# Kernel tuning notes

Hardware: AMD Instinct MI355X
Metric: run time of the kernel (lower is better)

The kernel has to match this reference:

```python
import jax, jax.numpy as jnp
import numpy as np

B, F, H, S, K, L, C = 128, 8192, 8192, 4, 32, 3, 100  # batch, encoded feats, hidden, segments, synapses/seg, hidden layers, classes


def setup_inputs() -> dict:
    key = jax.random.key(0)
    k1, k2, k3, k4, k5, k6 = jax.random.split(key, 6)
    # binary encoded input activations (thermometer-coded tabular features)
    x = jax.random.randint(k1, (B, F), 0, 2).astype(jnp.float32)
    # sign weights in {-1,+1} for each synapse of each segment of each neuron
    signs0 = jnp.where(jax.random.bernoulli(k2, 0.5, (S, H, K)), 1.0, -1.0).astype(jnp.float32)
    signsH = jnp.where(jax.random.bernoulli(k3, 0.5, (L - 1, S, H, K)), 1.0, -1.0).astype(jnp.float32)
    # synapse source indices (irregular connectivity)
    idx0 = jax.random.randint(k4, (S, H, K), 0, F, dtype=jnp.int32)
    idxH = jax.random.randint(k5, (L - 1, S, H, K), 0, H, dtype=jnp.int32)
    # per-layer output connection matrices [L, H, C]
    wout = jax.random.normal(k6, (L, H, C), dtype=jnp.float32) * 0.02
    return {"x": x, "signs0": signs0, "signsH": signsH, "wout": wout,
            "idx0": idx0, "idxH": idxH, "threshold": 8}


def _segment_layer(a, idx, signs, threshold):
    # a: [B, P] prev activations; idx/signs: [S, H, K]
    g = a[:, idx]                                  # [B, S, H, K] irregular gather
    z = jnp.einsum('bshk,shk->bsh', g, signs)      # per-segment summed input
    fired = jnp.any(z >= threshold, axis=1)        # OR over segments -> [B, H]
    return fired.astype(a.dtype)


def reference(x, signs0, signsH, wout, idx0, idxH, threshold):
    thr = jnp.float32(threshold)
    a = _segment_layer(x, idx0, signs0, thr)       # hidden layer 0
    acts = [a]
    for l in range(idxH.shape[0]):                 # remaining hidden layers (fixed small L)
        a = _segment_layer(a, idxH[l], signsH[l], thr)
        acts.append(a)
    # sum class votes from every hidden layer's output connection matrix
    out = jnp.einsum('lbh,lhc->bc', jnp.stack(acts, 0), wout)  # [B, C]
    return out
```

## Files before the change

### kernel.cpp

```cpp
#include <hip/hip_runtime.h>
#include <stdint.h>

#define B 128
#define F 8192
#define H 8192
#define S 4
#define K 32
#define L 3
#define C 100

__global__ void pack_x_kernel(const float* __restrict__ x, uint32_t* __restrict__ xP,
                              float* __restrict__ out) {
    const int zi = blockIdx.x * 128 + threadIdx.x;
    if (zi < B * C) out[zi] = 0.0f;

    const int b = threadIdx.x;
    const int wv = threadIdx.x >> 6;
    const int f0 = blockIdx.x * 8;
    const float4* xr = (const float4*)(x + (size_t)b * F + f0);
#pragma unroll
    for (int j = 0; j < 2; ++j) {
        const float4 v = xr[j];
        const uint64_t m0 = __ballot(v.x > 0.5f);
        const uint64_t m1 = __ballot(v.y > 0.5f);
        const uint64_t m2 = __ballot(v.z > 0.5f);
        const uint64_t m3 = __ballot(v.w > 0.5f);
        if ((threadIdx.x & 63) == 0) {
            const int f = f0 + 4 * j;
            uint32_t* lo = xP + (size_t)(2 * wv) * F;
            uint32_t* hi = xP + (size_t)(2 * wv + 1) * F;
            lo[f + 0] = (uint32_t)m0;  hi[f + 0] = (uint32_t)(m0 >> 32);
            lo[f + 1] = (uint32_t)m1;  hi[f + 1] = (uint32_t)(m1 >> 32);
            lo[f + 2] = (uint32_t)m2;  hi[f + 2] = (uint32_t)(m2 >> 32);
            lo[f + 3] = (uint32_t)m3;  hi[f + 3] = (uint32_t)(m3 >> 32);
        }
    }
}

__device__ __forceinline__ int load_threshold(const int* p) {
    int v = *p;
    if (v >= (1 << 23)) v = (int)__int_as_float(v);
    return v;
}

#define ISG_STRIDE 40

__device__ __forceinline__ void layer_body(const uint32_t* __restrict__ prevP,
                                           const int* __restrict__ idx,
                                           const float* __restrict__ signs,
                                           uint32_t* __restrict__ outP,
                                           const int thr, const int bid,
                                           uint32_t* tab, uint32_t* isg,
                                           uint32_t* fbuf) {
    const int tid  = threadIdx.x;
    const int lane = tid & 63;
    const int sw   = tid >> 6;
    const int w    = bid & 3;
    const int hg   = bid >> 2;
    const int h    = hg * 64 + lane;

    {
        const int4* src = (const int4*)(prevP + (size_t)w * H);
        int4* dst = (int4*)tab;
#pragma unroll
        for (int i = 0; i < 8; ++i)
            dst[i * 256 + tid] = src[i * 256 + tid];
    }
    {
        const int hrow = tid >> 2;
        const int k0   = (tid & 3) * 8;
#pragma unroll
        for (int s = 0; s < S; ++s) {
            const int4*   ib = (const int4*)(idx   + ((size_t)s * H + hg * 64) * K);
            const float4* sb = (const float4*)(signs + ((size_t)s * H + hg * 64) * K);
            const int4   ia = ib[2 * tid],  ic = ib[2 * tid + 1];
            const float4 sa = sb[2 * tid],  sc = sb[2 * tid + 1];
            uint4* dst = (uint4*)(isg + s * (64 * ISG_STRIDE) + hrow * ISG_STRIDE + k0);
            uint4 p0, p1;
            p0.x = (uint32_t)ia.x | ((uint32_t)__float_as_int(sa.x) & 0x80000000u);
            p0.y = (uint32_t)ia.y | ((uint32_t)__float_as_int(sa.y) & 0x80000000u);
            p0.z = (uint32_t)ia.z | ((uint32_t)__float_as_int(sa.z) & 0x80000000u);
            p0.w = (uint32_t)ia.w | ((uint32_t)__float_as_int(sa.w) & 0x80000000u);
            p1.x = (uint32_t)ic.x | ((uint32_t)__float_as_int(sc.x) & 0x80000000u);
            p1.y = (uint32_t)ic.y | ((uint32_t)__float_as_int(sc.y) & 0x80000000u);
            p1.z = (uint32_t)ic.z | ((uint32_t)__float_as_int(sc.z) & 0x80000000u);
            p1.w = (uint32_t)ic.w | ((uint32_t)__float_as_int(sc.w) & 0x80000000u);
            dst[0] = p0;
            dst[1] = p1;
        }
    }
    __syncthreads();

    uint32_t A[6] = {0, 0, 0, 0, 0, 0};
    uint32_t P[6] = {0, 0, 0, 0, 0, 0};
    const uint4* row4 = (const uint4*)(isg + sw * (64 * ISG_STRIDE) + lane * ISG_STRIDE);
#pragma unroll
    for (int c = 0; c < 4; ++c) {
        const uint4 r0 = row4[2 * c];
        const uint4 r1 = row4[2 * c + 1];
        const uint32_t iv[8] = {r0.x, r0.y, r0.z, r0.w, r1.x, r1.y, r1.z, r1.w};
        uint32_t a[8];
#pragma unroll
        for (int j = 0; j < 8; ++j) a[j] = tab[iv[j] & 0xFFFFu];
#pragma unroll
        for (int j = 0; j < 8; ++j) {
            const uint32_t pm = ~(uint32_t)((int32_t)iv[j] >> 31);
            uint32_t cc = a[j];
#pragma unroll
            for (int i = 0; i < 6; ++i) { const uint32_t t = A[i]; A[i] = t ^ cc; cc = t & cc; }
            cc = a[j] & pm;
#pragma unroll
            for (int i = 0; i < 6; ++i) { const uint32_t t = P[i]; P[i] = t ^ cc; cc = t & cc; }
        }
    }

    uint32_t Y[7];
    {
        uint32_t c = 0;
#pragma unroll
        for (int i = 0; i < 7; ++i) {
            const uint32_t ai = (i < 6) ? A[i] : 0u;
            const uint32_t bm = ((thr >> i) & 1) ? 0xFFFFFFFFu : 0u;
            const uint32_t t  = ai ^ bm;
            Y[i] = t ^ c;
            c = (ai & bm) | (t & c);
        }
    }
    uint32_t bw = 0;
#pragma unroll
    for (int i = 0; i < 7; ++i) {
        const uint32_t xx = (i >= 1) ? P[i - 1] : 0u;
        const uint32_t d  = xx ^ Y[i];
        bw = ((~xx) & Y[i]) | ((~d) & bw);
    }
    const uint32_t fired = ~bw;

    fbuf[sw * 64 + lane] = fired;
    __syncthreads();
    if (sw == 0) {
        const uint32_t f = fbuf[lane] | fbuf[64 + lane] |
                           fbuf[128 + lane] | fbuf[192 + lane];
        outP[(size_t)w * H + h] = f;
    }
}

__global__ void layer_kernel(const uint32_t* __restrict__ prevP,
                             const int* __restrict__ idx,
                             const float* __restrict__ signs,
                             uint32_t* __restrict__ outP,
                             const int* __restrict__ thrp) {
    __shared__ uint32_t tab[H];
    __shared__ uint32_t isg[S * 64 * ISG_STRIDE];
    __shared__ uint32_t fbuf[256];
    layer_body(prevP, idx, signs, outP, load_threshold(thrp), blockIdx.x,
               tab, isg, fbuf);
}

#define NHC 32
#define HCH (H / NHC)

__device__ __forceinline__ void final_body(const uint32_t* __restrict__ actP,
                                           const float* __restrict__ wout,
                                           float* __restrict__ out,
                                           const int item, const int lbeg,
                                           const int lend) {
    const int lane = threadIdx.x & 63;
    const int wid  = threadIdx.x >> 6;
    const int hc   = item & (NHC - 1);
    const int bg   = item / NHC;
    const int b    = bg * 4 + wid;
    const int w32  = b >> 5;
    const int bit  = b & 31;

    float acc0 = 0.0f, acc1 = 0.0f;
    const int c1 = 64 + lane;
    const bool c1v = (c1 < C);

    for (int l = lbeg; l <= lend; ++l) {
        const uint32_t* aT = actP + ((size_t)l * 4 + w32) * H;
        const float* wl = wout + (size_t)l * H * C;
        for (int r = 0; r < HCH / 64; ++r) {
            const int hbase = hc * HCH + r * 64;
            const uint32_t m = aT[hbase + lane];
            uint64_t hm = __ballot((m >> bit) & 1u);
            while (hm) {
                const int slot = __ffsll((unsigned long long)hm) - 1;
                hm &= hm - 1;
                const float* wr = wl + (size_t)(hbase + slot) * C;
                acc0 += wr[lane];
                if (c1v) acc1 += wr[c1];
            }
        }
    }
    atomicAdd(&out[b * C + lane], acc0);
    if (c1v) atomicAdd(&out[b * C + c1], acc1);
}

__global__ void layer2_final01_kernel(const uint32_t* __restrict__ prevP,
                                      const int* __restrict__ idx,
                                      const float* __restrict__ signs,
                                      uint32_t* __restrict__ outP,
                                      const int* __restrict__ thrp,
                                      const uint32_t* __restrict__ actP,
                                      const float* __restrict__ wout,
                                      float* __restrict__ out) {
    __shared__ uint32_t tab[H];
    __shared__ uint32_t isg[S * 64 * ISG_STRIDE];
    __shared__ uint32_t fbuf[256];
    if (blockIdx.x < 512) {
        layer_body(prevP, idx, signs, outP, load_threshold(thrp), blockIdx.x,
                   tab, isg, fbuf);
    } else {
        final_body(actP, wout, out, blockIdx.x - 512, 0, 1);
    }
}

__global__ void final2_kernel(const uint32_t* __restrict__ actP,
                              const float* __restrict__ wout,
                              float* __restrict__ out) {
    final_body(actP, wout, out, blockIdx.x, 2, 2);
}

extern "C" void kernel_launch(void* const* d_in, const int* in_sizes, int n_in,
                              void* d_out, int out_size, void* d_ws, size_t ws_size,
                              hipStream_t stream) {
    const float* x      = (const float*)d_in[0];
    const float* signs0 = (const float*)d_in[1];
    const float* signsH = (const float*)d_in[2];
    const float* wout   = (const float*)d_in[3];
    const int*   idx0   = (const int*)d_in[4];
    const int*   idxH   = (const int*)d_in[5];
    const int*   thr    = (const int*)d_in[6];
    float* out = (float*)d_out;

    uint32_t* xP   = (uint32_t*)d_ws;
    uint32_t* actP = xP + (size_t)4 * F;

    pack_x_kernel<<<1024, 128, 0, stream>>>(x, xP, out);

    layer_kernel<<<512, 256, 0, stream>>>(xP, idx0, signs0, actP, thr);
    layer_kernel<<<512, 256, 0, stream>>>(actP, idxH, signsH,
                                          actP + (size_t)4 * H, thr);
    layer2_final01_kernel<<<1536, 256, 0, stream>>>(
        actP + (size_t)4 * H,
        idxH + (size_t)S * H * K,
        signsH + (size_t)S * H * K,
        actP + (size_t)8 * H, thr,
        actP, wout, out);
    final2_kernel<<<1024, 256, 0, stream>>>(actP, wout, out);
}
```

Baseline: 134.1 us.

## Fuse per-layer output voting into the hidden-layer kernels and drop final pass

Each hidden-layer kernel now runs its own layer pass and then does the output voting for the previous layer in the same blocks. The old extra blocks and the separate final kernel go away. The last layer's votes are added straight from the fired bits of wave 0 with per-element atomics, removing one launch and one re-read of the activation bitmaps. The voting inner loop handles two set bits per iteration, and the input packing kernel handles four times more features per block. The trade-off is that voting now runs after the layer pass inside each block instead of in parallel blocks. The direct last-layer path may also cause heavy atomic contention on the output.

```diff
diff --git a/kernel.cpp b/kernel.cpp
--- a/kernel.cpp
+++ b/kernel.cpp
@@ -16,10 +16,9 @@
 
     const int b = threadIdx.x;
     const int wv = threadIdx.x >> 6;
-    const int f0 = blockIdx.x * 8;
+    const int f0 = blockIdx.x * 32;
     const float4* xr = (const float4*)(x + (size_t)b * F + f0);
-#pragma unroll
-    for (int j = 0; j < 2; ++j) {
+    for (int j = 0; j < 8; ++j) {
         const float4 v = xr[j];
         const uint64_t m0 = __ballot(v.x > 0.5f);
         const uint64_t m1 = __ballot(v.y > 0.5f);
@@ -45,13 +44,13 @@
 
 #define ISG_STRIDE 40
 
-__device__ __forceinline__ void layer_body(const uint32_t* __restrict__ prevP,
-                                           const int* __restrict__ idx,
-                                           const float* __restrict__ signs,
-                                           uint32_t* __restrict__ outP,
-                                           const int thr, const int bid,
-                                           uint32_t* tab, uint32_t* isg,
-                                           uint32_t* fbuf) {
+__device__ __forceinline__ uint32_t layer_body(const uint32_t* __restrict__ prevP,
+                                               const int* __restrict__ idx,
+                                               const float* __restrict__ signs,
+                                               uint32_t* __restrict__ outP,
+                                               const int thr, const int bid,
+                                               uint32_t* tab, uint32_t* isg,
+                                               uint32_t* fbuf) {
     const int tid  = threadIdx.x;
     const int lane = tid & 63;
     const int sw   = tid >> 6;
@@ -137,11 +136,13 @@
 
     fbuf[sw * 64 + lane] = fired;
     __syncthreads();
+    uint32_t f = 0;
     if (sw == 0) {
-        const uint32_t f = fbuf[lane] | fbuf[64 + lane] |
-                           fbuf[128 + lane] | fbuf[192 + lane];
+        f = fbuf[lane] | fbuf[64 + lane] |
+            fbuf[128 + lane] | fbuf[192 + lane];
         outP[(size_t)w * H + h] = f;
     }
+    return f;
 }
 
 __global__ void layer_kernel(const uint32_t* __restrict__ prevP,
@@ -156,18 +157,17 @@
                tab, isg, fbuf);
 }
 
-#define NHC 32
-#define HCH (H / NHC)
+#define FNHC 16
+#define FHCH (H / FNHC)
 
 __device__ __forceinline__ void final_body(const uint32_t* __restrict__ actP,
                                            const float* __restrict__ wout,
                                            float* __restrict__ out,
-                                           const int item, const int lbeg,
-                                           const int lend) {
+                                           const int item, const int l) {
     const int lane = threadIdx.x & 63;
     const int wid  = threadIdx.x >> 6;
-    const int hc   = item & (NHC - 1);
-    const int bg   = item / NHC;
+    const int hc   = item & (FNHC - 1);
+    const int bg   = item / FNHC;
     const int b    = bg * 4 + wid;
     const int w32  = b >> 5;
     const int bit  = b & 31;
@@ -176,49 +176,88 @@
     const int c1 = 64 + lane;
     const bool c1v = (c1 < C);
 
-    for (int l = lbeg; l <= lend; ++l) {
-        const uint32_t* aT = actP + ((size_t)l * 4 + w32) * H;
-        const float* wl = wout + (size_t)l * H * C;
-        for (int r = 0; r < HCH / 64; ++r) {
-            const int hbase = hc * HCH + r * 64;
-            const uint32_t m = aT[hbase + lane];
-            uint64_t hm = __ballot((m >> bit) & 1u);
+    const uint32_t* aT = actP + ((size_t)l * 4 + w32) * H;
+    const float* wl = wout + (size_t)l * H * C;
+    for (int r = 0; r < FHCH / 64; ++r) {
+        const int hbase = hc * FHCH + r * 64;
+        const uint32_t m = aT[hbase + lane];
+        uint64_t hm = __ballot((m >> bit) & 1u);
+        while (hm) {
+            const int s0 = __ffsll((unsigned long long)hm) - 1;
+            hm &= hm - 1;
+            const float* wr0 = wl + (size_t)(hbase + s0) * C;
+            if (hm) {
+                const int s1 = __ffsll((unsigned long long)hm) - 1;
+                hm &= hm - 1;
+                const float* wr1 = wl + (size_t)(hbase + s1) * C;
+                const float a0 = wr0[lane];
+                const float a1 = wr1[lane];
+                const float b0 = c1v ? wr0[c1] : 0.0f;
+                const float b1 = c1v ? wr1[c1] : 0.0f;
+                acc0 += a0 + a1;
+                acc1 += b0 + b1;
+            } else {
+                acc0 += wr0[lane];
+                if (c1v) acc1 += wr0[c1];
+            }
+        }
+    }
+    atomicAdd(&out[b * C + lane], acc0);
+    if (c1v) atomicAdd(&out[b * C + c1], acc1);
+}
+
+__global__ void layer1f_kernel(const uint32_t* __restrict__ prevP,
+                               const int* __restrict__ idx,
+                               const float* __restrict__ signs,
+                               uint32_t* __restrict__ outP,
+                               const int* __restrict__ thrp,
+                               const uint32_t* __restrict__ actP,
+                               const float* __restrict__ wout,
+                               float* __restrict__ out) {
+    __shared__ uint32_t tab[H];
+    __shared__ uint32_t isg[S * 64 * ISG_STRIDE];
+    __shared__ uint32_t fbuf[256];
+    layer_body(prevP, idx, signs, outP, load_threshold(thrp), blockIdx.x,
+               tab, isg, fbuf);
+    final_body(actP, wout, out, blockIdx.x, 0);
+}
+
+__global__ void layer2f_kernel(const uint32_t* __restrict__ prevP,
+                               const int* __restrict__ idx,
+                               const float* __restrict__ signs,
+                               uint32_t* __restrict__ outP,
+                               const int* __restrict__ thrp,
+                               const uint32_t* __restrict__ actP,
+                               const float* __restrict__ wout,
+                               float* __restrict__ out) {
+    __shared__ uint32_t tab[H];
+    __shared__ uint32_t isg[S * 64 * ISG_STRIDE];
+    __shared__ uint32_t fbuf[256];
+    const uint32_t f = layer_body(prevP, idx, signs, outP, load_threshold(thrp),
+                                  blockIdx.x, tab, isg, fbuf);
+    final_body(actP, wout, out, blockIdx.x, 1);
+
+    if ((threadIdx.x >> 6) == 0) {
+        const int lane = threadIdx.x & 63;
+        const int w    = blockIdx.x & 3;
+        const int hg   = blockIdx.x >> 2;
+        const float* w2 = wout + (size_t)2 * H * C;
+        const int c1 = 64 + lane;
+        const bool c1v = (c1 < C);
+#pragma unroll 1
+        for (int b = 0; b < 32; ++b) {
+            uint64_t hm = __ballot((f >> b) & 1u);
+            if (hm == 0ull) continue;
+            const int bb = w * 32 + b;
             while (hm) {
                 const int slot = __ffsll((unsigned long long)hm) - 1;
                 hm &= hm - 1;
-                const float* wr = wl + (size_t)(hbase + slot) * C;
-                acc0 += wr[lane];
-                if (c1v) acc1 += wr[c1];
+                const float* wr = w2 + (size_t)(hg * 64 + slot) * C;
+                atomicAdd(&out[bb * C + lane], wr[lane]);
+                if (c1v) atomicAdd(&out[bb * C + c1], wr[c1]);
             }
         }
     }
-    atomicAdd(&out[b * C + lane], acc0);
-    if (c1v) atomicAdd(&out[b * C + c1], acc1);
-}
-
-__global__ void layer2_final01_kernel(const uint32_t* __restrict__ prevP,
-                                      const int* __restrict__ idx,
-                                      const float* __restrict__ signs,
-                                      uint32_t* __restrict__ outP,
-                                      const int* __restrict__ thrp,
-                                      const uint32_t* __restrict__ actP,
-                                      const float* __restrict__ wout,
-                                      float* __restrict__ out) {
-    __shared__ uint32_t tab[H];
-    __shared__ uint32_t isg[S * 64 * ISG_STRIDE];
-    __shared__ uint32_t fbuf[256];
-    if (blockIdx.x < 512) {
-        layer_body(prevP, idx, signs, outP, load_threshold(thrp), blockIdx.x,
-                   tab, isg, fbuf);
-    } else {
-        final_body(actP, wout, out, blockIdx.x - 512, 0, 1);
-    }
-}
-
-__global__ void final2_kernel(const uint32_t* __restrict__ actP,
-                              const float* __restrict__ wout,
-                              float* __restrict__ out) {
-    final_body(actP, wout, out, blockIdx.x, 2, 2);
 }
 
 extern "C" void kernel_launch(void* const* d_in, const int* in_sizes, int n_in,
@@ -236,16 +275,17 @@
     uint32_t* xP   = (uint32_t*)d_ws;
     uint32_t* actP = xP + (size_t)4 * F;
 
-    pack_x_kernel<<<1024, 128, 0, stream>>>(x, xP, out);
+    pack_x_kernel<<<F / 32, 128, 0, stream>>>(x, xP, out);
 
     layer_kernel<<<512, 256, 0, stream>>>(xP, idx0, signs0, actP, thr);
-    layer_kernel<<<512, 256, 0, stream>>>(actP, idxH, signsH,
-                                          actP + (size_t)4 * H, thr);
-    layer2_final01_kernel<<<1536, 256, 0, stream>>>(
-        actP + (size_t)4 * H,
-        idxH + (size_t)S * H * K,
-        signsH + (size_t)S * H * K,
-        actP + (size_t)8 * H, thr,
-        actP, wout, out);
-    final2_kernel<<<1024, 256, 0, stream>>>(actP, wout, out);
-}
+
+    layer1f_kernel<<<512, 256, 0, stream>>>(actP, idxH, signsH,
+                                            actP + (size_t)4 * H, thr,
+                                            actP, wout, out);
+
+    layer2f_kernel<<<512, 256, 0, stream>>>(actP + (size_t)4 * H,
+                                            idxH + (size_t)S * H * K,
+                                            signsH + (size_t)S * H * K,
+                                            actP + (size_t)8 * H, thr,
+                                            actP, wout, out);
+}
```

Measured after the change: 126.7 us. -5.5%, faster.
